# Kernel optimization log

Measured on AMD Instinct MI355X. Metric: run time of the kernel, lower is better.

The kernel has to match this reference:

```python
import jax, jax.numpy as jnp
import numpy as np

N_NODES = 20000
N_EDGES = 320000
N_GRAPHS = 64


def gat_conv(x, src, dst, W, a_src, a_dst, bias, heads, ch, concat):
    # x: [N, F_in]; W: [F_in, heads*ch]; a_src/a_dst: [heads, ch]
    N = x.shape[0]
    h = (x @ W).reshape(N, heads, ch)                       # [N, H, C]
    alpha_s = jnp.sum(h * a_src, axis=-1)                   # [N, H]
    alpha_d = jnp.sum(h * a_dst, axis=-1)                   # [N, H]
    e = jax.nn.leaky_relu(alpha_s[src] + alpha_d[dst], 0.2) # [E, H]
    # segment softmax over incoming edges of each destination node
    m = jax.ops.segment_max(e, dst, num_segments=N)         # [N, H]
    ex = jnp.exp(e - m[dst])
    denom = jax.ops.segment_sum(ex, dst, num_segments=N)    # [N, H]
    alpha = ex / (denom[dst] + 1e-16)                       # [E, H]
    msg = h[src] * alpha[:, :, None]                        # [E, H, C]
    out = jax.ops.segment_sum(msg, dst, num_segments=N)     # [N, H, C]
    out = out.reshape(N, heads * ch) if concat else out.mean(axis=1)
    return out + bias, alpha


def setup_inputs() -> dict:
    key = jax.random.key(0)
    ks = jax.random.split(key, 24)
    dim_in, md, dim_out = 8, 64, 128
    hid = md * 4  # 256
    p = lambda k, shape: jax.random.normal(k, shape, dtype=jnp.float32) * 0.1
    inp = {
        "x_ppi": jax.random.normal(ks[0], (N_NODES, dim_in), dtype=jnp.float32),
        "ppi_edge_index": jax.random.randint(ks[1], (2, N_EDGES), 0, N_NODES),
        "ppi_batch": jnp.sort(jax.random.randint(ks[2], (N_NODES,), 0, N_GRAPHS)),
        # GATConv 1: dim_in -> 64, heads=4, concat
        "W1": p(ks[3], (dim_in, 4 * md)), "a_src1": p(ks[4], (4, md)), "a_dst1": p(ks[5], (4, md)), "b_gat1": jnp.zeros((hid,), jnp.float32),
        "lw1": p(ks[6], (dim_in, hid)), "lb1": jnp.zeros((hid,), jnp.float32),
        # GATConv 2: 256 -> 64, heads=4, concat
        "W2": p(ks[7], (hid, 4 * md)), "a_src2": p(ks[8], (4, md)), "a_dst2": p(ks[9], (4, md)), "b_gat2": jnp.zeros((hid,), jnp.float32),
        "lw2": p(ks[10], (hid, hid)), "lb2": jnp.zeros((hid,), jnp.float32),
        # GATConv 3: 256 -> 128, heads=6, concat=False (mean)
        "W3": p(ks[11], (hid, 6 * dim_out)), "a_src3": p(ks[12], (6, dim_out)), "a_dst3": p(ks[13], (6, dim_out)), "b_gat3": jnp.zeros((dim_out,), jnp.float32),
        "lw3": p(ks[14], (hid, dim_out)), "lb3": jnp.zeros((dim_out,), jnp.float32),
        # BatchNorm1d(dim_out), training-mode batch statistics
        "bn_gamma": jnp.ones((dim_out,), jnp.float32), "bn_beta": jnp.zeros((dim_out,), jnp.float32),
    }
    return inp


def reference(x_ppi, ppi_edge_index, ppi_batch,
              W1, a_src1, a_dst1, b_gat1, lw1, lb1,
              W2, a_src2, a_dst2, b_gat2, lw2, lb2,
              W3, a_src3, a_dst3, b_gat3, lw3, lb3,
              bn_gamma, bn_beta):
    src, dst = ppi_edge_index[0], ppi_edge_index[1]
    g1, _ = gat_conv(x_ppi, src, dst, W1, a_src1, a_dst1, b_gat1, heads=4, ch=64, concat=True)
    x = jax.nn.relu(g1 + x_ppi @ lw1 + lb1)
    g2, _ = gat_conv(x, src, dst, W2, a_src2, a_dst2, b_gat2, heads=4, ch=64, concat=True)
    x = jax.nn.relu(g2 + x @ lw2 + lb2)
    x_res = x @ lw3 + lb3
    g3, att = gat_conv(x, src, dst, W3, a_src3, a_dst3, b_gat3, heads=6, ch=128, concat=False)
    x = g3 + x_res
    x = jax.nn.relu(x)
    # BatchNorm1d, training mode (biased variance, eps=1e-5)
    mu = x.mean(axis=0)
    var = jnp.mean((x - mu) ** 2, axis=0)
    x = (x - mu) * jax.lax.rsqrt(var + 1e-5) * bn_gamma + bn_beta
    # global max pool over graphs
    pooled = jax.ops.segment_max(x, ppi_batch, num_segments=N_GRAPHS)
    return pooled, att
```

## Files before the change

kernel.cpp:

```cpp
#include <hip/hip_runtime.h>
#include <hip/hip_bf16.h>
#include <math.h>

#define N_NODES 20000
#define N_EDGES 320000
#define N_GRAPHS 64

typedef __bf16 bf16_t;
typedef bf16_t bf16x8 __attribute__((ext_vector_type(8)));
typedef bf16_t bf16x4 __attribute__((ext_vector_type(4)));
typedef bf16_t bf16x2 __attribute__((ext_vector_type(2)));
typedef float f32x4 __attribute__((ext_vector_type(4)));
typedef float f32x2 __attribute__((ext_vector_type(2)));

__global__ void hist_k(const int* __restrict__ dst, int* __restrict__ deg, int E) {
    int e = blockIdx.x * 256 + threadIdx.x;
    if (e < E) atomicAdd(&deg[dst[e]], 1);
}

__global__ __launch_bounds__(1024) void scan_k(const int* __restrict__ deg,
                                               int* __restrict__ offs,
                                               int* __restrict__ cursor, int n) {
    __shared__ int s_ws[16];
    int tid = threadIdx.x;
    int lane = tid & 63, w = tid >> 6;
    int carry = 0;
    for (int base = 0; base < n; base += 1024) {
        int i = base + tid;
        int v = (i < n) ? deg[i] : 0;
        int x = v;
        #pragma unroll
        for (int off = 1; off < 64; off <<= 1) {
            int t = __shfl_up(x, off);
            if (lane >= off) x += t;
        }
        if (lane == 63) s_ws[w] = x;
        __syncthreads();
        if (tid < 16) {
            int y = s_ws[tid];
            #pragma unroll
            for (int off = 1; off < 16; off <<= 1) {
                int t = __shfl_up(y, off);
                if (tid >= off) y += t;
            }
            s_ws[tid] = y;
        }
        __syncthreads();
        int wbase = (w > 0) ? s_ws[w - 1] : 0;
        int ex = carry + wbase + x - v;
        if (i < n) { offs[i] = ex; cursor[i] = ex; }
        carry += s_ws[15];
        __syncthreads();
    }
    if (tid == 0) offs[n] = carry;
}

__global__ void scatter_k(const int* __restrict__ src, const int* __restrict__ dst,
                          int* __restrict__ cursor, int* __restrict__ csr_src,
                          int* __restrict__ csr_eid, int E) {
    int e = blockIdx.x * 256 + threadIdx.x;
    if (e < E) {
        int d = dst[e];
        int p = atomicAdd(&cursor[d], 1);
        csr_src[p] = src[e];
        csr_eid[p] = e;
    }
}

__global__ __launch_bounds__(256) void wt_k(const float* __restrict__ W,
                                            bf16_t* __restrict__ Bt, int K, int N) {
    __shared__ float t[32][33];
    int k0 = blockIdx.y * 32, n0 = blockIdx.x * 32;
    int tx = threadIdx.x & 31, ty = threadIdx.x >> 5;
    for (int i = ty; i < 32; i += 8) t[i][tx] = W[(size_t)(k0 + i) * N + n0 + tx];
    __syncthreads();
    for (int i = ty; i < 32; i += 8)
        Bt[(size_t)(n0 + i) * K + k0 + tx] = (bf16_t)t[tx][i];
}

__global__ void w3s_k(const float* __restrict__ W3, const float* __restrict__ lw3,
                      bf16_t* __restrict__ Bt) {
    int id = blockIdx.x * 256 + threadIdx.x;
    if (id >= 128 * 1792) return;
    int n = id / 1792, k = id - n * 1792;
    float v;
    if (k < 1536) {
        int h = k >> 8, c = k & 255;
        v = W3[(size_t)c * 768 + h * 128 + n] * (1.f / 6.f);
    } else {
        int c = k - 1536;
        v = lw3[(size_t)c * 128 + n];
    }
    Bt[id] = (bf16_t)v;
}

__global__ void b40_k(const float* __restrict__ W1, const float* __restrict__ lw1,
                      float* __restrict__ B) {
    int id = blockIdx.x * 256 + threadIdx.x;
    if (id >= 40 * 256) return;
    int k = id >> 8, n = id & 255;
    float v;
    if (k < 32) {
        int h = k >> 3, c = k & 7;
        v = ((n >> 6) == h) ? W1[(size_t)c * 256 + n] : 0.f;
    } else {
        int c = k - 32;
        v = lw1[(size_t)c * 256 + n];
    }
    B[id] = v;
}

__global__ void va_k(const float* __restrict__ W, const float* __restrict__ a_s,
                     const float* __restrict__ a_d, float* __restrict__ Va,
                     float* __restrict__ Vd, int H, int C) {
    int k = blockIdx.x;
    int lane = threadIdx.x;
    const float* wr = W + (size_t)k * H * C;
    for (int h = 0; h < H; ++h) {
        float sa = 0.f, sd = 0.f;
        for (int c = lane; c < C; c += 64) {
            float wv = wr[h * C + c];
            sa += wv * a_s[h * C + c];
            sd += wv * a_d[h * C + c];
        }
        #pragma unroll
        for (int m = 32; m; m >>= 1) { sa += __shfl_xor(sa, m); sd += __shfl_xor(sd, m); }
        if (lane == 0) { Va[k * H + h] = sa; Vd[k * H + h] = sd; }
    }
}

__global__ void addb_k(const float* __restrict__ a, const float* __restrict__ b,
                       float* __restrict__ o, int n) {
    int i = blockIdx.x * 256 + threadIdx.x;
    if (i < n) o[i] = a[i] + b[i];
}

template <typename OUT>
__global__ __launch_bounds__(256) void gemm_k(const float* __restrict__ A,
                                              const float* __restrict__ B,
                                              OUT* __restrict__ C,
                                              const float* __restrict__ bias,
                                              int M, int N, int K, int relu) {
    __shared__ float As[16][65];
    __shared__ float Bs[16][64];
    int tid = threadIdx.x;
    int tx = tid & 15, ty = tid >> 4;
    int row0 = blockIdx.y * 64, col0 = blockIdx.x * 64;
    float acc[4][4] = {};
    for (int k0 = 0; k0 < K; k0 += 16) {
        #pragma unroll
        for (int i = 0; i < 4; ++i) {
            int idx = tid + i * 256;
            int m = idx >> 4, kk = idx & 15;
            int gm = row0 + m, gk = k0 + kk;
            As[kk][m] = (gm < M && gk < K) ? A[(size_t)gm * K + gk] : 0.f;
        }
        #pragma unroll
        for (int i = 0; i < 4; ++i) {
            int idx = tid + i * 256;
            int kk = idx >> 6, n = idx & 63;
            int gk = k0 + kk, gn = col0 + n;
            Bs[kk][n] = (gk < K && gn < N) ? B[(size_t)gk * N + gn] : 0.f;
        }
        __syncthreads();
        #pragma unroll
        for (int kk = 0; kk < 16; ++kk) {
            float a[4], b[4];
            #pragma unroll
            for (int i = 0; i < 4; ++i) a[i] = As[kk][ty * 4 + i];
            #pragma unroll
            for (int j = 0; j < 4; ++j) b[j] = Bs[kk][tx * 4 + j];
            #pragma unroll
            for (int i = 0; i < 4; ++i)
                #pragma unroll
                for (int j = 0; j < 4; ++j) acc[i][j] += a[i] * b[j];
        }
        __syncthreads();
    }
    #pragma unroll
    for (int i = 0; i < 4; ++i) {
        int gm = row0 + ty * 4 + i;
        if (gm >= M) continue;
        #pragma unroll
        for (int j = 0; j < 4; ++j) {
            int gn = col0 + tx * 4 + j;
            if (gn < N) {
                float r = acc[i][j] + (bias ? bias[gn] : 0.f);
                if (relu) r = fmaxf(r, 0.f);
                C[(size_t)gm * N + gn] = (OUT)r;
            }
        }
    }
}

template <typename OUT>
__global__ __launch_bounds__(256) void gemm_bf16_k(
    const bf16_t* __restrict__ A, const bf16_t* __restrict__ Bt,
    OUT* __restrict__ C, const float* __restrict__ bias, int M, int N, int K,
    const float* __restrict__ asv, const float* __restrict__ adv,
    float* __restrict__ as_o, float* __restrict__ ad_o, int H, int Ch, int relu) {
    __shared__ bf16_t As[128][40];
    __shared__ bf16_t Bs[128][40];
    int tid = threadIdx.x;
    int row0 = blockIdx.y * 128, col0 = blockIdx.x * 128;
    int wave = tid >> 6, lane = tid & 63, quad = lane >> 4, l16 = lane & 15;
    int wm = wave >> 1, wn = wave & 1;
    f32x4 acc[4][4] = {};
    int sr = tid >> 2;
    int sc = (tid & 3) * 8;
    for (int k0 = 0; k0 < K; k0 += 32) {
        #pragma unroll
        for (int half = 0; half < 2; ++half) {
            int r = sr + half * 64;
            int gm = row0 + r;
            bf16x8 v = {};
            if (gm < M) v = *(const bf16x8*)&A[(size_t)gm * K + k0 + sc];
            *(bf16x8*)&As[r][sc] = v;
            int gn = col0 + r;
            bf16x8 w = {};
            if (gn < N) w = *(const bf16x8*)&Bt[(size_t)gn * K + k0 + sc];
            *(bf16x8*)&Bs[r][sc] = w;
        }
        __syncthreads();
        bf16x8 af[4], bfr[4];
        #pragma unroll
        for (int i = 0; i < 4; ++i) {
            af[i] = *(const bf16x8*)&As[wm * 64 + i * 16 + l16][quad * 8];
            bfr[i] = *(const bf16x8*)&Bs[wn * 64 + i * 16 + l16][quad * 8];
        }
        #pragma unroll
        for (int i = 0; i < 4; ++i)
            #pragma unroll
            for (int j = 0; j < 4; ++j)
                acc[i][j] = __builtin_amdgcn_mfma_f32_16x16x32_bf16(af[i], bfr[j],
                                                                   acc[i][j], 0, 0, 0);
        __syncthreads();
    }
    #pragma unroll
    for (int i = 0; i < 4; ++i) {
        int base_m = row0 + wm * 64 + i * 16 + quad * 4;
        #pragma unroll
        for (int j = 0; j < 4; ++j) {
            int gn = col0 + wn * 64 + j * 16 + l16;
            float bv = bias ? bias[gn] : 0.f;
            #pragma unroll
            for (int r = 0; r < 4; ++r) {
                int gm = base_m + r;
                if (gm < M) {
                    float rr = acc[i][j][r] + bv;
                    if (relu) rr = fmaxf(rr, 0.f);
                    C[(size_t)gm * N + gn] = (OUT)rr;
                }
            }
        }
    }
    if (asv) {
        int hd = (col0 + wn * 64) / Ch;
        float av[4], dv[4];
        #pragma unroll
        for (int j = 0; j < 4; ++j) {
            int ca = col0 + wn * 64 + j * 16 + l16;
            av[j] = asv[ca];
            dv[j] = adv[ca];
        }
        #pragma unroll
        for (int i = 0; i < 4; ++i) {
            float sp[4] = {}, sd[4] = {};
            #pragma unroll
            for (int j = 0; j < 4; ++j)
                #pragma unroll
                for (int r = 0; r < 4; ++r) {
                    sp[r] += acc[i][j][r] * av[j];
                    sd[r] += acc[i][j][r] * dv[j];
                }
            #pragma unroll
            for (int m = 1; m < 16; m <<= 1)
                #pragma unroll
                for (int r = 0; r < 4; ++r) {
                    sp[r] += __shfl_xor(sp[r], m);
                    sd[r] += __shfl_xor(sd[r], m);
                }
            if (l16 == 0) {
                #pragma unroll
                for (int r = 0; r < 4; ++r) {
                    int gm = row0 + wm * 64 + i * 16 + quad * 4 + r;
                    if (gm < M) {
                        as_o[gm * H + hd] = sp[r];
                        ad_o[gm * H + hd] = sd[r];
                    }
                }
            }
        }
    }
}

__device__ __forceinline__ float leaky02(float v) { return v > 0.f ? v : 0.2f * v; }

__global__ void asad1_k(const float* __restrict__ x, const float* __restrict__ Va,
                        const float* __restrict__ Vd, float* __restrict__ as_,
                        float* __restrict__ ad_, int N) {
    int idx = blockIdx.x * 256 + threadIdx.x;
    if (idx >= N * 4) return;
    int j = idx >> 2, h = idx & 3;
    const float* xr = x + (size_t)j * 8;
    float sa = 0.f, sd = 0.f;
    #pragma unroll
    for (int c = 0; c < 8; ++c) {
        sa += xr[c] * Va[c * 4 + h];
        sd += xr[c] * Vd[c * 4 + h];
    }
    as_[idx] = sa;
    ad_[idx] = sd;
}

__global__ void asad3_k(const bf16_t* __restrict__ xb, const float* __restrict__ Va,
                        const float* __restrict__ Vd, float* __restrict__ as_,
                        float* __restrict__ ad_) {
    int j = blockIdx.x;
    int lane = threadIdx.x;
    bf16x4 v = *(const bf16x4*)&xb[(size_t)j * 256 + lane * 4];
    float sa[6] = {}, sd[6] = {};
    #pragma unroll
    for (int i = 0; i < 4; ++i) {
        int k = lane * 4 + i;
        float xv = (float)v[i];
        #pragma unroll
        for (int h = 0; h < 6; ++h) {
            sa[h] += xv * Va[k * 6 + h];
            sd[h] += xv * Vd[k * 6 + h];
        }
    }
    #pragma unroll
    for (int h = 0; h < 6; ++h) {
        float a = sa[h], d = sd[h];
        #pragma unroll
        for (int m = 32; m; m >>= 1) { a += __shfl_xor(a, m); d += __shfl_xor(d, m); }
        if (lane == 0) { as_[j * 6 + h] = a; ad_[j * 6 + h] = d; }
    }
}

__global__ __launch_bounds__(256) void agg_z1_k(
    const float* __restrict__ x, const float* __restrict__ as_,
    const float* __restrict__ ad_, const int* __restrict__ offs,
    const int* __restrict__ csr_src, float* __restrict__ z1) {
    int j = blockIdx.x * 4 + (threadIdx.x >> 6);
    int t = threadIdx.x & 63;
    int e_l = t >> 3, c = t & 7;
    int o0 = offs[j], deg = offs[j + 1] - o0;
    float adj0 = ad_[j * 4 + 0], adj1 = ad_[j * 4 + 1];
    float adj2 = ad_[j * 4 + 2], adj3 = ad_[j * 4 + 3];
    float acc[4] = {}, ws[4] = {};
    for (int e0 = 0; e0 < deg; e0 += 8) {
        int ne = min(8, deg - e0);
        if (e_l < ne) {
            int s = csr_src[o0 + e0 + e_l];
            float xv = x[(size_t)s * 8 + c];
            f32x4 a = *(const f32x4*)&as_[s * 4];
            float w0 = __expf(leaky02(a[0] + adj0));
            float w1 = __expf(leaky02(a[1] + adj1));
            float w2 = __expf(leaky02(a[2] + adj2));
            float w3 = __expf(leaky02(a[3] + adj3));
            acc[0] += w0 * xv; acc[1] += w1 * xv;
            acc[2] += w2 * xv; acc[3] += w3 * xv;
            ws[0] += w0; ws[1] += w1; ws[2] += w2; ws[3] += w3;
        }
    }
    #pragma unroll
    for (int m = 8; m < 64; m <<= 1)
        #pragma unroll
        for (int h = 0; h < 4; ++h) {
            acc[h] += __shfl_xor(acc[h], m);
            ws[h] += __shfl_xor(ws[h], m);
        }
    if (e_l == 0) {
        #pragma unroll
        for (int h = 0; h < 4; ++h)
            z1[(size_t)j * 40 + h * 8 + c] = acc[h] / (ws[h] + 1e-16f);
        z1[(size_t)j * 40 + 32 + c] = x[(size_t)j * 8 + c];
    }
}

__global__ __launch_bounds__(256) void agg_concat_k(
    const bf16_t* __restrict__ h, const float* __restrict__ as_,
    const float* __restrict__ ad_, const int* __restrict__ offs,
    const int* __restrict__ csr_src, const float* __restrict__ lin,
    const float* __restrict__ bgat, bf16_t* __restrict__ xb) {
    int j = blockIdx.x;
    int tid = threadIdx.x;
    int o0 = offs[j], deg = offs[j + 1] - o0;
    __shared__ int s_src[64];
    __shared__ float s_adj[4];
    __shared__ float s_ws[8][4];
    __shared__ float s_inv[4];
    __shared__ float s_red[8][256];
    if (tid < 4) s_adj[tid] = ad_[j * 4 + tid];
    int g = tid >> 5;
    int u = tid & 31;
    int myh = u >> 3;
    const char* hbase = (const char*)h + u * 16;
    f32x4 acc0 = {}, acc1 = {};
    float wsum = 0.f;
    for (int e0 = 0; e0 < deg; e0 += 64) {
        int ne = min(64, deg - e0);
        if (tid < ne) s_src[tid] = csr_src[o0 + e0 + tid];
        __syncthreads();
        float adj = s_adj[myh];
        #pragma unroll 2
        for (int e = g; e < ne; e += 8) {
            int s = s_src[e];
            float w = __expf(leaky02(as_[s * 4 + myh] + adj));
            bf16x8 v = *(const bf16x8*)(hbase + (size_t)s * 512);
            wsum += w;
            #pragma unroll
            for (int i = 0; i < 4; ++i) acc0[i] += w * (float)v[i];
            #pragma unroll
            for (int i = 0; i < 4; ++i) acc1[i] += w * (float)v[4 + i];
        }
        __syncthreads();
    }
    if ((u & 7) == 0) s_ws[g][myh] = wsum;
    *(f32x4*)&s_red[g][u * 8] = acc0;
    *(f32x4*)&s_red[g][u * 8 + 4] = acc1;
    __syncthreads();
    if (tid < 4) {
        float d = 0.f;
        #pragma unroll
        for (int g2 = 0; g2 < 8; ++g2) d += s_ws[g2][tid];
        s_inv[tid] = 1.f / (d + 1e-16f);
    }
    __syncthreads();
    {
        int c = tid;
        float s = 0.f;
        #pragma unroll
        for (int g2 = 0; g2 < 8; ++g2) s += s_red[g2][c];
        float v = fmaxf(s * s_inv[c >> 6] + bgat[c] + lin[(size_t)j * 256 + c], 0.f);
        xb[(size_t)j * 256 + c] = (bf16_t)v;
    }
}

__global__ __launch_bounds__(192) void agg_z3_k(
    const bf16_t* __restrict__ xb, const float* __restrict__ as_,
    const float* __restrict__ ad_, const int* __restrict__ offs,
    const int* __restrict__ csr_src, const int* __restrict__ csr_eid,
    bf16_t* __restrict__ z, float* __restrict__ att) {
    int j = blockIdx.x;
    int tid = threadIdx.x;
    int o0 = offs[j], deg = offs[j + 1] - o0;
    __shared__ float s_adj[6];
    __shared__ int s_src[64];
    __shared__ float s_w[64 * 6];
    __shared__ float s_inv[6];
    if (tid < 6) s_adj[tid] = ad_[j * 6 + tid];
    __syncthreads();
    int h = tid >> 5;
    int c = tid & 31;
    const char* xbase = (const char*)xb + c * 16;
    f32x4 a0 = {}, a1 = {};
    float wsum = 0.f;
    for (int e0 = 0; e0 < deg; e0 += 64) {
        int ne = min(64, deg - e0);
        #pragma unroll
        for (int base = 0; base < 2; ++base) {
            int idx = tid + base * 192;
            if (idx < ne * 6) {
                int e = idx / 6, hh = idx - e * 6;
                int s = csr_src[o0 + e0 + e];
                if (hh == 0) s_src[e] = s;
                s_w[idx] = __expf(leaky02(as_[s * 6 + hh] + s_adj[hh]));
            }
        }
        __syncthreads();
        #pragma unroll 4
        for (int e = 0; e < ne; ++e) {
            int s = s_src[e];
            float w = s_w[e * 6 + h];
            bf16x8 v = *(const bf16x8*)(xbase + (size_t)s * 512);
            wsum += w;
            #pragma unroll
            for (int i = 0; i < 4; ++i) a0[i] += w * (float)v[i];
            #pragma unroll
            for (int i = 0; i < 4; ++i) a1[i] += w * (float)v[4 + i];
        }
        __syncthreads();
    }
    float inv = 1.f / (wsum + 1e-16f);
    {
        bf16x8 o;
        #pragma unroll
        for (int i = 0; i < 4; ++i) o[i] = (bf16_t)(a0[i] * inv);
        #pragma unroll
        for (int i = 0; i < 4; ++i) o[4 + i] = (bf16_t)(a1[i] * inv);
        *(bf16x8*)&z[(size_t)j * 1792 + h * 256 + c * 8] = o;
    }
    if (tid < 32)
        *(bf16x8*)&z[(size_t)j * 1792 + 1536 + tid * 8] =
            *(const bf16x8*)&xb[(size_t)j * 256 + tid * 8];
    if (c == 0) s_inv[h] = inv;
    __syncthreads();
    for (int idx = tid; idx < deg * 6; idx += 192) {
        int e = idx / 6, hh = idx - e * 6;
        int p = o0 + e;
        int s = csr_src[p];
        att[(size_t)csr_eid[p] * 6 + hh] =
            __expf(leaky02(as_[s * 6 + hh] + s_adj[hh])) * s_inv[hh];
    }
}

__global__ void bn_stats_k(const float* __restrict__ y, float* __restrict__ sums, int N) {
    int c = threadIdx.x;
    float s = 0.f, q = 0.f;
    for (int r = blockIdx.x; r < N; r += gridDim.x) {
        float v = y[(size_t)r * 128 + c];
        s += v;
        q += v * v;
    }
    atomicAdd(&sums[c], s);
    atomicAdd(&sums[128 + c], q);
}
__global__ void bn_scale_k(const float* __restrict__ sums, const float* __restrict__ gamma,
                           const float* __restrict__ beta, float* __restrict__ scale,
                           float* __restrict__ shift, int N) {
    int c = threadIdx.x;
    float mu = sums[c] / (float)N;
    float var = fmaxf(sums[128 + c] / (float)N - mu * mu, 0.f);
    float inv = rsqrtf(var + 1e-5f) * gamma[c];
    scale[c] = inv;
    shift[c] = beta[c] - mu * inv;
}

__device__ __forceinline__ unsigned f2key(float f) {
    unsigned b = __float_as_uint(f);
    return (b & 0x80000000u) ? ~b : (b | 0x80000000u);
}
__global__ void pool_init_k(unsigned* __restrict__ pool_u) {
    int i = blockIdx.x * 256 + threadIdx.x;
    if (i < N_GRAPHS * 128) pool_u[i] = f2key(-3.402823466e38f * 2.0f);
}
__global__ void norm_pool_k(const float* __restrict__ y, const float* __restrict__ scale,
                            const float* __restrict__ shift, const int* __restrict__ batch,
                            unsigned* __restrict__ pool_u, int N) {
    int idx = blockIdx.x * 256 + threadIdx.x;
    if (idx >= N * 128) return;
    int n = idx >> 7, c = idx & 127;
    float v = y[idx] * scale[c] + shift[c];
    atomicMax(&pool_u[batch[n] * 128 + c], f2key(v));
}
__global__ void pool_write_k(const unsigned* __restrict__ pool_u, float* __restrict__ out) {
    int i = blockIdx.x * 256 + threadIdx.x;
    if (i < N_GRAPHS * 128) {
        unsigned u = pool_u[i];
        unsigned b = (u & 0x80000000u) ? (u & 0x7FFFFFFFu) : ~u;
        out[i] = __uint_as_float(b);
    }
}

extern "C" void kernel_launch(void* const* d_in, const int* in_sizes, int n_in,
                              void* d_out, int out_size, void* d_ws, size_t ws_size,
                              hipStream_t stream) {
    const int N = N_NODES, E = N_EDGES;
    const float* x_ppi = (const float*)d_in[0];
    const int* edge = (const int*)d_in[1];
    const int* batch = (const int*)d_in[2];
    const float* W1 = (const float*)d_in[3];
    const float* a_src1 = (const float*)d_in[4];
    const float* a_dst1 = (const float*)d_in[5];
    const float* b_gat1 = (const float*)d_in[6];
    const float* lw1 = (const float*)d_in[7];
    const float* lb1 = (const float*)d_in[8];
    const float* W2 = (const float*)d_in[9];
    const float* a_src2 = (const float*)d_in[10];
    const float* a_dst2 = (const float*)d_in[11];
    const float* b_gat2 = (const float*)d_in[12];
    const float* lw2 = (const float*)d_in[13];
    const float* lb2 = (const float*)d_in[14];
    const float* W3 = (const float*)d_in[15];
    const float* a_src3 = (const float*)d_in[16];
    const float* a_dst3 = (const float*)d_in[17];
    const float* b_gat3 = (const float*)d_in[18];
    const float* lw3 = (const float*)d_in[19];
    const float* lb3 = (const float*)d_in[20];
    const float* bn_gamma = (const float*)d_in[21];
    const float* bn_beta = (const float*)d_in[22];

    const int* src = edge;
    const int* dst = edge + E;

    size_t off = 0;
    auto alloc = [&](size_t bytes) {
        size_t o = off;
        off = (off + bytes + 255) & ~(size_t)255;
        return o;
    };
    char* ws = (char*)d_ws;
    bf16_t* xb = (bf16_t*)(ws + alloc((size_t)N * 256 * 2));
    bf16_t* zbig = (bf16_t*)(ws + alloc((size_t)N * 1792 * 2));
    bf16_t* hb = zbig;
    bf16_t* z3 = zbig;
    float* lin = (float*)(ws + alloc((size_t)N * 256 * 4));
    float* z1 = (float*)(ws + alloc((size_t)N * 40 * 4));
    float* as_ = (float*)(ws + alloc((size_t)N * 6 * 4));
    float* ad_ = (float*)(ws + alloc((size_t)N * 6 * 4));
    int* deg = (int*)(ws + alloc((size_t)(N + 1) * 4));
    int* offs = (int*)(ws + alloc((size_t)(N + 1) * 4));
    int* cursor = (int*)(ws + alloc((size_t)(N + 1) * 4));
    int* csr_src = (int*)(ws + alloc((size_t)E * 4));
    int* csr_eid = (int*)(ws + alloc((size_t)E * 4));
    bf16_t* Wt2 = (bf16_t*)(ws + alloc((size_t)256 * 256 * 2));
    bf16_t* lwt2 = (bf16_t*)(ws + alloc((size_t)256 * 256 * 2));
    bf16_t* Bt3s = (bf16_t*)(ws + alloc((size_t)128 * 1792 * 2));
    float* B40 = (float*)(ws + alloc((size_t)40 * 256 * 4));
    float* Va1 = (float*)(ws + alloc(8 * 4 * 4));
    float* Vd1 = (float*)(ws + alloc(8 * 4 * 4));
    float* Va3 = (float*)(ws + alloc(256 * 6 * 4));
    float* Vd3 = (float*)(ws + alloc(256 * 6 * 4));
    float* bias1s = (float*)(ws + alloc(256 * 4));
    float* bias3s = (float*)(ws + alloc(128 * 4));
    float* bn_sums = (float*)(ws + alloc(256 * 4));
    float* bn_scale = (float*)(ws + alloc(128 * 4));
    float* bn_shift = (float*)(ws + alloc(128 * 4));
    unsigned* pool_u = (unsigned*)(ws + alloc((size_t)N_GRAPHS * 128 * 4));

    float* out_pool = (float*)d_out;
    float* out_att = (float*)d_out + N_GRAPHS * 128;

    hipMemsetAsync(deg, 0, (size_t)N * 4, stream);
    hist_k<<<(E + 255) / 256, 256, 0, stream>>>(dst, deg, E);
    scan_k<<<1, 1024, 0, stream>>>(deg, offs, cursor, N);
    scatter_k<<<(E + 255) / 256, 256, 0, stream>>>(src, dst, cursor, csr_src, csr_eid, E);
    wt_k<<<dim3(8, 8), 256, 0, stream>>>(W2, Wt2, 256, 256);
    wt_k<<<dim3(8, 8), 256, 0, stream>>>(lw2, lwt2, 256, 256);
    w3s_k<<<896, 256, 0, stream>>>(W3, lw3, Bt3s);
    b40_k<<<40, 256, 0, stream>>>(W1, lw1, B40);
    va_k<<<8, 64, 0, stream>>>(W1, a_src1, a_dst1, Va1, Vd1, 4, 64);
    va_k<<<256, 64, 0, stream>>>(W3, a_src3, a_dst3, Va3, Vd3, 6, 128);
    addb_k<<<1, 256, 0, stream>>>(lb1, b_gat1, bias1s, 256);
    addb_k<<<1, 128, 0, stream>>>(lb3, b_gat3, bias3s, 128);

    asad1_k<<<(N * 4 + 255) / 256, 256, 0, stream>>>(x_ppi, Va1, Vd1, as_, ad_, N);
    agg_z1_k<<<N / 4, 256, 0, stream>>>(x_ppi, as_, ad_, offs, csr_src, z1);
    gemm_k<bf16_t><<<dim3(4, 313), 256, 0, stream>>>(z1, B40, xb, bias1s, N, 256, 40, 1);

    gemm_bf16_k<bf16_t><<<dim3(2, 157), 256, 0, stream>>>(xb, Wt2, hb, nullptr, N, 256, 256,
                                                          a_src2, a_dst2, as_, ad_, 4, 64, 0);
    gemm_bf16_k<float><<<dim3(2, 157), 256, 0, stream>>>(xb, lwt2, lin, lb2, N, 256, 256,
                                                         nullptr, nullptr, nullptr, nullptr,
                                                         0, 1, 0);
    agg_concat_k<<<N, 256, 0, stream>>>(hb, as_, ad_, offs, csr_src, lin, b_gat2, xb);

    asad3_k<<<N, 64, 0, stream>>>(xb, Va3, Vd3, as_, ad_);
    agg_z3_k<<<N, 192, 0, stream>>>(xb, as_, ad_, offs, csr_src, csr_eid, z3, out_att);
    float* y = lin;
    gemm_bf16_k<float><<<dim3(1, 157), 256, 0, stream>>>(z3, Bt3s, y, bias3s, N, 128, 1792,
                                                         nullptr, nullptr, nullptr, nullptr,
                                                         0, 1, 1);

    hipMemsetAsync(bn_sums, 0, 256 * 4, stream);
    bn_stats_k<<<160, 128, 0, stream>>>(y, bn_sums, N);
    bn_scale_k<<<1, 128, 0, stream>>>(bn_sums, bn_gamma, bn_beta, bn_scale, bn_shift, N);

    pool_init_k<<<(N_GRAPHS * 128 + 255) / 256, 256, 0, stream>>>(pool_u);
    norm_pool_k<<<((size_t)N * 128 + 255) / 256, 256, 0, stream>>>(y, bn_scale, bn_shift, batch,
                                                                   pool_u, N);
    pool_write_k<<<(N_GRAPHS * 128 + 255) / 256, 256, 0, stream>>>(pool_u, out_pool);
}
```

Baseline: 494.7 us.

## Split-K the final layer-3 GEMM with atomic accumulation

```diff
diff --git a/kernel.cpp b/kernel.cpp
--- a/kernel.cpp
+++ b/kernel.cpp
@@ -291,6 +291,72 @@
                 }
             }
         }
+    }
+}
+
+__global__ __launch_bounds__(256) void gemm_bf16_sk_k(
+    const bf16_t* __restrict__ A, const bf16_t* __restrict__ Bt,
+    float* __restrict__ C, int M, int N, int K, int Kc) {
+    __shared__ bf16_t As[128][40];
+    __shared__ bf16_t Bs[128][40];
+    int tid = threadIdx.x;
+    int row0 = blockIdx.y * 128;
+    int kb = blockIdx.x * Kc;
+    int ke = min(K, kb + Kc);
+    int wave = tid >> 6, lane = tid & 63, quad = lane >> 4, l16 = lane & 15;
+    int wm = wave >> 1, wn = wave & 1;
+    f32x4 acc[4][4] = {};
+    int sr = tid >> 2;
+    int sc = (tid & 3) * 8;
+    for (int k0 = kb; k0 < ke; k0 += 32) {
+        #pragma unroll
+        for (int half = 0; half < 2; ++half) {
+            int r = sr + half * 64;
+            int gm = row0 + r;
+            bf16x8 v = {};
+            if (gm < M) v = *(const bf16x8*)&A[(size_t)gm * K + k0 + sc];
+            *(bf16x8*)&As[r][sc] = v;
+            bf16x8 w = {};
+            if (r < N) w = *(const bf16x8*)&Bt[(size_t)r * K + k0 + sc];
+            *(bf16x8*)&Bs[r][sc] = w;
+        }
+        __syncthreads();
+        bf16x8 af[4], bfr[4];
+        #pragma unroll
+        for (int i = 0; i < 4; ++i) {
+            af[i] = *(const bf16x8*)&As[wm * 64 + i * 16 + l16][quad * 8];
+            bfr[i] = *(const bf16x8*)&Bs[wn * 64 + i * 16 + l16][quad * 8];
+        }
+        #pragma unroll
+        for (int i = 0; i < 4; ++i)
+            #pragma unroll
+            for (int j = 0; j < 4; ++j)
+                acc[i][j] = __builtin_amdgcn_mfma_f32_16x16x32_bf16(af[i], bfr[j],
+                                                                   acc[i][j], 0, 0, 0);
+        __syncthreads();
+    }
+    #pragma unroll
+    for (int i = 0; i < 4; ++i) {
+        int base_m = row0 + wm * 64 + i * 16 + quad * 4;
+        #pragma unroll
+        for (int j = 0; j < 4; ++j) {
+            int gn = wn * 64 + j * 16 + l16;
+            if (gn >= N) continue;
+            #pragma unroll
+            for (int r = 0; r < 4; ++r) {
+                int gm = base_m + r;
+                if (gm < M) atomicAdd(&C[(size_t)gm * N + gn], acc[i][j][r]);
+            }
+        }
+    }
+}
+
+__global__ void finrelu_k(float* __restrict__ y, const float* __restrict__ bias,
+                          int total) {
+    int i = blockIdx.x * 256 + threadIdx.x;
+    if (i < total) {
+        int c = i & 127;
+        y[i] = fmaxf(y[i] + bias[c], 0.f);
     }
 }
 
@@ -648,12 +714,12 @@
                                                          0, 1, 0);
     agg_concat_k<<<N, 256, 0, stream>>>(hb, as_, ad_, offs, csr_src, lin, b_gat2, xb);
 
+    float* y = lin;
     asad3_k<<<N, 64, 0, stream>>>(xb, Va3, Vd3, as_, ad_);
     agg_z3_k<<<N, 192, 0, stream>>>(xb, as_, ad_, offs, csr_src, csr_eid, z3, out_att);
-    float* y = lin;
-    gemm_bf16_k<float><<<dim3(1, 157), 256, 0, stream>>>(z3, Bt3s, y, bias3s, N, 128, 1792,
-                                                         nullptr, nullptr, nullptr, nullptr,
-                                                         0, 1, 1);
+    hipMemsetAsync(y, 0, (size_t)N * 128 * 4, stream);
+    gemm_bf16_sk_k<<<dim3(8, 157), 256, 0, stream>>>(z3, Bt3s, y, N, 128, 1792, 224);
+    finrelu_k<<<((size_t)N * 128 + 255) / 256, 256, 0, stream>>>(y, bias3s, N * 128);
 
     hipMemsetAsync(bn_sums, 0, 256 * 4, stream);
     bn_stats_k<<<160, 128, 0, stream>>>(y, bn_sums, N);
```

After: 512.3 us. 3.6% more time.
